# Optimization experiments

Measured on AMD Instinct MI355X. Metric: run time of the kernel, lower is better.

The kernel has to match this reference:

```python
import jax, jax.numpy as jnp
import numpy as np

# pywt 'db4' decomposition filters
DEC_LO = np.array([-0.010597401784997278, 0.032883011666982945, 0.030841381835986965,
                   -0.18703481171888114, -0.02798376941698385, 0.6308807679295904,
                   0.7148465705525415, 0.23037781330885523], dtype=np.float32)
DEC_HI = np.array([(-1.0) ** (k + 1) * DEC_LO[len(DEC_LO) - 1 - k] for k in range(len(DEC_LO))],
                  dtype=np.float32)
FLEN = 8
LEVELS = 4
# lax conv does cross-correlation; pywt dwt is convolution -> reverse the filters.
# Kernel shape [out_ch=2 (lo,hi), in_ch=1, width=8]
KERNEL = jnp.stack([jnp.asarray(DEC_LO[::-1].copy()), jnp.asarray(DEC_HI[::-1].copy())])[:, None, :]


def _dwt_step(x):
    """One pywt-compatible DWT level with 'symmetric' extension.
    x: [N, 1, L] -> (cA [N,1,Lo], cD [N,1,Lo]) with Lo = floor((L+FLEN-1)/2).
    pywt: extend by FLEN-1 each side, full-conv, take every 2nd sample starting at 1.
    Equivalent: slice ext[1:], stride-2 valid cross-correlation with reversed filter."""
    ext = jnp.pad(x, ((0, 0), (0, 0), (FLEN - 1, FLEN - 1)), mode='symmetric')[:, :, 1:]
    out = jax.lax.conv_general_dilated(ext, KERNEL, window_strides=(2,), padding='VALID',
                                       dimension_numbers=('NCH', 'OIH', 'NCH'))
    return out[:, 0:1, :], out[:, 1:2, :]


def setup_inputs() -> dict:
    key = jax.random.key(0)
    trajectory = jax.random.normal(key, (16, 4096, 256), dtype=jnp.float32)
    return {"trajectory": trajectory}


def reference(trajectory) -> jnp.ndarray:
    """Batched multi-level DWT (pywt.wavedec, db4, symmetric, level=4),
    each coefficient band zero-padded to `timesteps`.
    Returns [batch, timesteps, levels+1, features]; band axis ordered
    [cA4, cD4, cD3, cD2, cD1] exactly as pywt.wavedec returns them.
    (Original torch code stored these values in a dict; values are identical.)"""
    B, T, F = trajectory.shape
    # vectorize all (batch, feature) signals together: [B*F, 1, T]
    x = trajectory.transpose(0, 2, 1).reshape(B * F, 1, T)
    details = []
    cur = x
    for _ in range(LEVELS):
        cur, cD = _dwt_step(cur)
        details.append(cD)
    bands = [cur] + details[::-1]  # [cA4, cD4, cD3, cD2, cD1]
    # zero-pad each band at the end to length T (matches _pad_coefficients)
    padded = [jnp.pad(c[:, 0, :], ((0, 0), (0, T - c.shape[-1]))) for c in bands]
    stacked = jnp.stack(padded, axis=1)  # [B*F, LEVELS+1, T]
    return stacked.reshape(B, F, LEVELS + 1, T).transpose(0, 3, 2, 1)  # [B, T, LEVELS+1, F]
```

## Files before the change

kernel.cpp:

```cpp
#include <hip/hip_runtime.h>


namespace {
constexpr int T_LEN = 4096;
constexpr int F_DIM = 256;
constexpr int NB    = 5;
constexpr int L1 = 2051, L2 = 1029, L3 = 518, L4 = 262;
}

__device__ __constant__ float RLO[8] = {
     0.23037781330885523f,   0.7148465705525415f,   0.6308807679295904f,
    -0.02798376941698385f,  -0.18703481171888114f,  0.030841381835986965f,
     0.032883011666982945f, -0.010597401784997278f };

__device__ __constant__ float RHI[8] = {
    -0.010597401784997278f, -0.032883011666982945f, 0.030841381835986965f,
     0.18703481171888114f,  -0.02798376941698385f, -0.6308807679295904f,
     0.7148465705525415f,   -0.23037781330885523f };

__device__ __host__ constexpr int refl(int i, int L) {
    return (i < 0) ? (-1 - i) : ((i >= L) ? (2 * L - 1 - i) : i);
}

__device__ __forceinline__ void nt_store(float* p, float v) {
    __builtin_nontemporal_store(v, p);
}

__device__ __forceinline__ void zero_pass(float* __restrict__ outb, int k)
{
    const int o1 = 32 * k, o2 = 16 * k, o3 = 8 * k, o4 = 4 * k;
    const int lv1 = max(0, min(32, L1 - o1));
    const int lv2 = max(0, min(16, L2 - o2));
    const int lv3 = max(0, min(8,  L3 - o3));
    const int lv4 = max(0, min(4,  L4 - o4));
    for (int r = lv1; r < 32; ++r) nt_store(outb + ((size_t)(o1 + r) * NB + 4) * F_DIM, 0.f);
    for (int r = lv2; r < 16; ++r) nt_store(outb + ((size_t)(o2 + r) * NB + 3) * F_DIM, 0.f);
    #pragma unroll
    for (int r = 0; r < 16; ++r)   nt_store(outb + ((size_t)(o2 + 2048 + r) * NB + 3) * F_DIM, 0.f);
    for (int r = lv3; r < 8; ++r)  nt_store(outb + ((size_t)(o3 + r) * NB + 2) * F_DIM, 0.f);
    #pragma unroll
    for (int j = 1; j < 4; ++j)
        #pragma unroll
        for (int r = 0; r < 8; ++r)
            nt_store(outb + ((size_t)(o3 + 1024 * j + r) * NB + 2) * F_DIM, 0.f);
    for (int r = lv4; r < 4; ++r) {
        nt_store(outb + ((size_t)(o4 + r) * NB + 1) * F_DIM, 0.f);
        nt_store(outb + ((size_t)(o4 + r) * NB + 0) * F_DIM, 0.f);
    }
    #pragma unroll
    for (int j = 1; j < 8; ++j)
        #pragma unroll
        for (int r = 0; r < 4; ++r) {
            nt_store(outb + ((size_t)(o4 + 512 * j + r) * NB + 1) * F_DIM, 0.f);
            nt_store(outb + ((size_t)(o4 + 512 * j + r) * NB + 0) * F_DIM, 0.f);
        }
}

template<int KX>
__device__ __forceinline__ void cascade(const float* __restrict__ inb,
                                        float* __restrict__ outb, int krt)
{
    constexpr bool EX = (KX >= 0);
    constexpr bool DP = (KX == 65);
    constexpr int N1 = DP ? 82 : 74, N2 = DP ? 38 : 34, N3 = DP ? 16 : 14;
    constexpr int OWN1 = DP ? 50 : 42, OWN2 = DP ? 22 : 18, OWN3 = DP ? 8 : 6;
    constexpr int R1LO = (KX == 0) ? 42 : (KX == 1) ? 10 : 0;
    constexpr int R1HI = (KX == 64) ? 45 : (KX == 65) ? 21 : N1;
    constexpr int R2LO = (KX == 0) ? 18 : (KX == 1) ? 2 : 0;
    constexpr int R2HI = (KX == 64) ? 23 : (KX == 65) ? 11 : N2;
    constexpr int R3LO = (KX == 0) ? 6 : 0;
    constexpr int R3HI = (KX == 64) ? 12 : (KX == 65) ? 6 : N3;
    constexpr int MHI  = (KX == 65) ? 2 : 4;

    const int k   = EX ? KX : krt;
    const int t1b = 32 * k - (DP ? 50 : 42);
    const int t2b = 16 * k - (DP ? 22 : 18);
    const int t3b = 8 * k  - (DP ? 8  : 6);

    float A[N1], B[N2], C[N3];

    float xw[8];
    #pragma unroll
    for (int j = 0; j < 8; ++j) {
        int g = 2 * (t1b + R1LO) - 6 + j;
        if (EX) g = refl(g, T_LEN);
        xw[j] = inb[(size_t)g * F_DIM];
    }
    #pragma unroll
    for (int r1 = R1LO; r1 < R1HI; ++r1) {
        float a = 0.f, d = 0.f;
        #pragma unroll
        for (int j = 0; j < 8; ++j) { a = fmaf(xw[j], RLO[j], a); d = fmaf(xw[j], RHI[j], d); }
        A[r1] = a;
        const int t1 = t1b + r1;
        if (r1 >= OWN1)
            nt_store(outb + ((size_t)t1 * NB + 4) * F_DIM, d);
        if (r1 + 1 < R1HI) {
            #pragma unroll
            for (int j = 0; j < 6; ++j) xw[j] = xw[j + 2];
            int g6 = 2 * t1 + 2, g7 = 2 * t1 + 3;
            if (EX) { g6 = refl(g6, T_LEN); g7 = refl(g7, T_LEN); }
            xw[6] = inb[(size_t)g6 * F_DIM];
            xw[7] = inb[(size_t)g7 * F_DIM];
        }
    }

    #pragma unroll
    for (int r2 = R2LO; r2 < R2HI; ++r2) {
        float a = 0.f, d = 0.f;
        #pragma unroll
        for (int j = 0; j < 8; ++j) {
            const int i1 = EX ? (refl(2 * (t2b + r2) - 6 + j, L1) - t1b) : (2 * r2 + j);
            const float v = A[i1];
            a = fmaf(v, RLO[j], a); d = fmaf(v, RHI[j], d);
        }
        B[r2] = a;
        if (r2 >= OWN2)
            nt_store(outb + ((size_t)(t2b + r2) * NB + 3) * F_DIM, d);
    }

    #pragma unroll
    for (int r3 = R3LO; r3 < R3HI; ++r3) {
        float a = 0.f, d = 0.f;
        #pragma unroll
        for (int j = 0; j < 8; ++j) {
            const int i2 = EX ? (refl(2 * (t3b + r3) - 6 + j, L2) - t2b) : (2 * r3 + j);
            const float v = B[i2];
            a = fmaf(v, RLO[j], a); d = fmaf(v, RHI[j], d);
        }
        C[r3] = a;
        if (r3 >= OWN3)
            nt_store(outb + ((size_t)(t3b + r3) * NB + 2) * F_DIM, d);
    }

    #pragma unroll
    for (int m = 0; m < MHI; ++m) {
        float a = 0.f, d = 0.f;
        #pragma unroll
        for (int j = 0; j < 8; ++j) {
            const int i3 = EX ? (refl(2 * (4 * k + m) - 6 + j, L3) - t3b) : (2 * m + j);
            const float v = C[i3];
            a = fmaf(v, RLO[j], a); d = fmaf(v, RHI[j], d);
        }
        const int t4 = 4 * k + m;
        nt_store(outb + ((size_t)t4 * NB + 1) * F_DIM, d);
        nt_store(outb + ((size_t)t4 * NB + 0) * F_DIM, a);
    }
}

extern "C" __global__ __launch_bounds__(256)
void dwt_fused(const float* __restrict__ in, float* __restrict__ out)
{
    const int f   = threadIdx.x;
    const int per = gridDim.x >> 3;
    const int wg  = (int)(blockIdx.x & 7) * per + (int)(blockIdx.x >> 3);
    const int b   = wg >> 7;
    const int k   = wg & 127;

    float* outb = out + (size_t)b * T_LEN * NB * F_DIM + f;
    zero_pass(outb, k);
    if (k >= 66) return;

    const float* inb = in + (size_t)b * T_LEN * F_DIM + f;
    switch (k) {
        case 0:  cascade<0 >(inb, outb, k); break;
        case 1:  cascade<1 >(inb, outb, k); break;
        case 64: cascade<64>(inb, outb, k); break;
        case 65: cascade<65>(inb, outb, k); break;
        default: cascade<-1>(inb, outb, k); break;
    }
}

extern "C" void kernel_launch(void* const* d_in, const int* in_sizes, int n_in,
                              void* d_out, int out_size, void* d_ws, size_t ws_size,
                              hipStream_t stream)
{
    const float* traj = (const float*)d_in[0];
    float* out = (float*)d_out;
    hipLaunchKernelGGL(dwt_fused, dim3(16 * 128), dim3(F_DIM), 0, stream, traj, out);
}
```

Measured before the change: 71.50 us.

## Move zero padding to idle workgroups with contiguous vectorized row stores

Zero-padding of the output bands used to be spread across all workgroups as strided scalar stores, one column per thread. Now the compute workgroups (j<66) only run the cascade. The remaining 62 workgroups per batch each zero a contiguous span of time rows, where the band tail sits contiguously at the start of each [NB,F] row. Those zeros go out as 16-byte nontemporal vector stores, which is meant to cut store-instruction count and use full lines. The risk is load imbalance: zero-fill blocks write many rows while compute blocks skip the zeroing work entirely.

```diff
diff --git a/kernel.cpp b/kernel.cpp
--- a/kernel.cpp
+++ b/kernel.cpp
@@ -7,6 +7,8 @@
 constexpr int NB    = 5;
 constexpr int L1 = 2051, L2 = 1029, L3 = 518, L4 = 262;
 }
+
+typedef float f32x4 __attribute__((ext_vector_type(4)));
 
 __device__ __constant__ float RLO[8] = {
      0.23037781330885523f,   0.7148465705525415f,   0.6308807679295904f,
@@ -26,34 +28,20 @@
     __builtin_nontemporal_store(v, p);
 }
 
-__device__ __forceinline__ void zero_pass(float* __restrict__ outb, int k)
+template<int Z>
+__device__ __forceinline__ void fill_zeros(float* __restrict__ outB,
+                                           int t0, int t1, int tid)
 {
-    const int o1 = 32 * k, o2 = 16 * k, o3 = 8 * k, o4 = 4 * k;
-    const int lv1 = max(0, min(32, L1 - o1));
-    const int lv2 = max(0, min(16, L2 - o2));
-    const int lv3 = max(0, min(8,  L3 - o3));
-    const int lv4 = max(0, min(4,  L4 - o4));
-    for (int r = lv1; r < 32; ++r) nt_store(outb + ((size_t)(o1 + r) * NB + 4) * F_DIM, 0.f);
-    for (int r = lv2; r < 16; ++r) nt_store(outb + ((size_t)(o2 + r) * NB + 3) * F_DIM, 0.f);
-    #pragma unroll
-    for (int r = 0; r < 16; ++r)   nt_store(outb + ((size_t)(o2 + 2048 + r) * NB + 3) * F_DIM, 0.f);
-    for (int r = lv3; r < 8; ++r)  nt_store(outb + ((size_t)(o3 + r) * NB + 2) * F_DIM, 0.f);
-    #pragma unroll
-    for (int j = 1; j < 4; ++j)
+    const f32x4 z4 = {0.f, 0.f, 0.f, 0.f};
+    for (int t = t0; t < t1; ++t) {
+        float* row = outB + (size_t)t * NB * F_DIM;
         #pragma unroll
-        for (int r = 0; r < 8; ++r)
-            nt_store(outb + ((size_t)(o3 + 1024 * j + r) * NB + 2) * F_DIM, 0.f);
-    for (int r = lv4; r < 4; ++r) {
-        nt_store(outb + ((size_t)(o4 + r) * NB + 1) * F_DIM, 0.f);
-        nt_store(outb + ((size_t)(o4 + r) * NB + 0) * F_DIM, 0.f);
+        for (int c0 = 0; c0 < Z * F_DIM; c0 += 4 * F_DIM) {
+            const int c = c0 + tid * 4;
+            if (c < Z * F_DIM)
+                __builtin_nontemporal_store(z4, (f32x4*)(row + c));
+        }
     }
-    #pragma unroll
-    for (int j = 1; j < 8; ++j)
-        #pragma unroll
-        for (int r = 0; r < 4; ++r) {
-            nt_store(outb + ((size_t)(o4 + 512 * j + r) * NB + 1) * F_DIM, 0.f);
-            nt_store(outb + ((size_t)(o4 + 512 * j + r) * NB + 0) * F_DIM, 0.f);
-        }
 }
 
 template<int KX>
@@ -151,23 +139,42 @@
 extern "C" __global__ __launch_bounds__(256)
 void dwt_fused(const float* __restrict__ in, float* __restrict__ out)
 {
-    const int f   = threadIdx.x;
+    const int tid = threadIdx.x;
     const int per = gridDim.x >> 3;
     const int wg  = (int)(blockIdx.x & 7) * per + (int)(blockIdx.x >> 3);
     const int b   = wg >> 7;
-    const int k   = wg & 127;
+    const int j   = wg & 127;
 
-    float* outb = out + (size_t)b * T_LEN * NB * F_DIM + f;
-    zero_pass(outb, k);
-    if (k >= 66) return;
+    float* outB = out + (size_t)b * T_LEN * NB * F_DIM;
 
-    const float* inb = in + (size_t)b * T_LEN * F_DIM + f;
-    switch (k) {
-        case 0:  cascade<0 >(inb, outb, k); break;
-        case 1:  cascade<1 >(inb, outb, k); break;
-        case 64: cascade<64>(inb, outb, k); break;
-        case 65: cascade<65>(inb, outb, k); break;
-        default: cascade<-1>(inb, outb, k); break;
+    if (j < 66) {
+        const float* inb = in + (size_t)b * T_LEN * F_DIM + tid;
+        float* outb = outB + tid;
+        switch (j) {
+            case 0:  cascade<0 >(inb, outb, j); break;
+            case 1:  cascade<1 >(inb, outb, j); break;
+            case 64: cascade<64>(inb, outb, j); break;
+            case 65: cascade<65>(inb, outb, j); break;
+            default: cascade<-1>(inb, outb, j); break;
+        }
+    } else {
+        const int slot = j - 66;
+        if (slot < 2) {
+            const int t0 = 262 + slot * 128;
+            fill_zeros<2>(outB, t0, t0 + 128, tid);
+        } else if (slot < 8) {
+            const int i = slot - 2;
+            const int t0 = 518 + i * 86;
+            fill_zeros<3>(outB, t0, (t0 + 86 < L2) ? t0 + 86 : L2, tid);
+        } else if (slot < 24) {
+            const int i = slot - 8;
+            const int t0 = 1029 + i * 64;
+            fill_zeros<4>(outB, t0, (t0 + 64 < L1) ? t0 + 64 : L1, tid);
+        } else {
+            const int i = slot - 24;
+            const int t0 = 2051 + i * 54;
+            fill_zeros<5>(outB, t0, (t0 + 54 < T_LEN) ? t0 + 54 : T_LEN, tid);
+        }
     }
 }
 
```

New measurement: 71.35 us. No clear change (-0.2%).
